# Kernel optimization log

Hardware: AMD Instinct MI355X
Metric: run time of the kernel (lower is better)

## Reference

```python
import jax, jax.numpy as jnp
import numpy as np

Y_DIM = 2
Z_DIM = 128
EPS = 1e-08


def setup_inputs() -> dict:
    key = jax.random.key(0)
    k1, k2, k3, k4 = jax.random.split(key, 4)
    b, n, m, x_dim = 8, 1024, 2048, 1
    c = Y_DIM + 1
    x = jax.random.normal(k1, (b, n, x_dim), dtype=jnp.float32)
    y = jax.random.normal(k2, (b, n, Y_DIM), dtype=jnp.float32)
    t = jax.random.normal(k3, (b, m, x_dim), dtype=jnp.float32)
    # learned params
    sigma = jnp.zeros((c,), dtype=jnp.float32)  # log(length_scale=1) = 0
    W = jax.random.normal(k4, (Z_DIM, c), dtype=jnp.float32) * 0.05
    b_fc = jnp.zeros((Z_DIM,), dtype=jnp.float32)
    return {"x": x, "y": y, "t": t, "sigma": sigma, "W": W, "b_fc": b_fc}


def reference(x, y, t, sigma, W, b_fc):
    # rbf_kernel: diff summed over x_dim -> (b, n, m)
    diff = jnp.sum(t[:, None, :, :] - x[:, :, None, :], axis=-1)  # (b,n,m)
    scale = jnp.exp(sigma)  # (c,)
    # kernel: (b,n,m,c)
    kernel = jnp.exp(-0.5 * (diff[..., None] / scale) ** 2)
    # z = [density=1, y] broadcast-multiplied by kernel, summed over n
    b_, n_, _ = y.shape
    feats = jnp.concatenate([jnp.ones((b_, n_, 1), dtype=y.dtype), y], axis=-1)  # (b,n,c)
    z = jnp.einsum("bnc,bnmc->bmc", feats, kernel)  # (b,m,c)
    density = z[..., :1]
    normalized = z[..., 1:] / (density + EPS)
    z = jnp.concatenate([density, normalized], axis=-1)  # (b,m,c)
    return z @ W.T + b_fc  # (b,m,z_dim)
```

## Files before the change

### kernel.cpp

```cpp
#include <hip/hip_runtime.h>
#include <hip/hip_bf16.h>

constexpr int B  = 8;
constexpr int N  = 1024;
constexpr int M  = 2048;
constexpr int ZD = 128;
constexpr int JPW = 2;
constexpr int JPB = 4 * JPW;
constexpr float EPS = 1e-8f;
constexpr float LOG2E = 1.4426950408889634f;

__global__ __launch_bounds__(256, 8) void encoder_fused(
    const float* __restrict__ x,
    const float* __restrict__ y,
    const float* __restrict__ t,
    const float* __restrict__ sigma,
    const float* __restrict__ W,
    const float* __restrict__ bfc,
    float* __restrict__ out)
{
    __shared__ float sx[N];
    __shared__ float sy1[N];
    __shared__ float sy2[N];

    const int blk  = blockIdx.x;
    const int b    = blk / (M / JPB);
    const int jt   = blk % (M / JPB);
    const int tid  = threadIdx.x;
    const int wave = tid >> 6;
    const int lane = tid & 63;

    for (int i = tid; i < N; i += 256) {
        sx[i] = x[b * N + i];
        float2 yv = reinterpret_cast<const float2*>(y)[b * N + i];
        sy1[i] = yv.x;
        sy2[i] = yv.y;
    }
    __syncthreads();

    const float s0 = sigma[0], s1 = sigma[1], s2 = sigma[2];
    const float q0 = -0.5f * LOG2E * __builtin_amdgcn_exp2f(-2.0f * s0 * LOG2E);
    const float q1 = -0.5f * LOG2E * __builtin_amdgcn_exp2f(-2.0f * s1 * LOG2E);
    const float q2 = -0.5f * LOG2E * __builtin_amdgcn_exp2f(-2.0f * s2 * LOG2E);

    const int j0 = jt * JPB + wave * JPW;
    const float ta = t[b * M + j0];
    const float tb = t[b * M + j0 + 1];

    float z0a = 0.f, z1a = 0.f, z2a = 0.f;
    float z0b = 0.f, z1b = 0.f, z2b = 0.f;

    if (s0 == s1 && s1 == s2) {
#pragma unroll
        for (int k = 0; k < N / 64; ++k) {
            const int i = k * 64 + lane;
            const float xi = sx[i], y1 = sy1[i], y2 = sy2[i];
            const float da = ta - xi, db = tb - xi;
            const float ea = __builtin_amdgcn_exp2f(da * da * q0);
            const float eb = __builtin_amdgcn_exp2f(db * db * q0);
            z0a += ea;  z1a = fmaf(y1, ea, z1a);  z2a = fmaf(y2, ea, z2a);
            z0b += eb;  z1b = fmaf(y1, eb, z1b);  z2b = fmaf(y2, eb, z2b);
        }
    } else {
#pragma unroll
        for (int k = 0; k < N / 64; ++k) {
            const int i = k * 64 + lane;
            const float xi = sx[i], y1 = sy1[i], y2 = sy2[i];
            const float da = ta - xi, db = tb - xi;
            const float da2 = da * da, db2 = db * db;
            z0a += __builtin_amdgcn_exp2f(da2 * q0);
            z1a = fmaf(y1, __builtin_amdgcn_exp2f(da2 * q1), z1a);
            z2a = fmaf(y2, __builtin_amdgcn_exp2f(da2 * q2), z2a);
            z0b += __builtin_amdgcn_exp2f(db2 * q0);
            z1b = fmaf(y1, __builtin_amdgcn_exp2f(db2 * q1), z1b);
            z2b = fmaf(y2, __builtin_amdgcn_exp2f(db2 * q2), z2b);
        }
    }

#pragma unroll
    for (int off = 32; off; off >>= 1) {
        z0a += __shfl_xor(z0a, off);
        z1a += __shfl_xor(z1a, off);
        z2a += __shfl_xor(z2a, off);
        z0b += __shfl_xor(z0b, off);
        z1b += __shfl_xor(z1b, off);
        z2b += __shfl_xor(z2b, off);
    }

    const float inva = 1.0f / (z0a + EPS);
    const float a1 = z1a * inva, a2 = z2a * inva;
    const float invb = 1.0f / (z0b + EPS);
    const float b1 = z1b * invb, b2 = z2b * invb;

    const int k0 = lane * 2;
    const float w00 = W[k0 * 3 + 0], w01 = W[k0 * 3 + 1], w02 = W[k0 * 3 + 2];
    const float w10 = W[(k0 + 1) * 3 + 0], w11 = W[(k0 + 1) * 3 + 1], w12 = W[(k0 + 1) * 3 + 2];
    const float bf0 = bfc[k0], bf1 = bfc[k0 + 1];

    float2 oa, ob;
    oa.x = fmaf(z0a, w00, fmaf(a1, w01, fmaf(a2, w02, bf0)));
    oa.y = fmaf(z0a, w10, fmaf(a1, w11, fmaf(a2, w12, bf1)));
    ob.x = fmaf(z0b, w00, fmaf(b1, w01, fmaf(b2, w02, bf0)));
    ob.y = fmaf(z0b, w10, fmaf(b1, w11, fmaf(b2, w12, bf1)));

    reinterpret_cast<float2*>(out)[(size_t)(b * M + j0) * (ZD / 2) + lane]       = oa;
    reinterpret_cast<float2*>(out)[(size_t)(b * M + j0 + 1) * (ZD / 2) + lane]   = ob;
}

extern "C" void kernel_launch(void* const* d_in, const int* in_sizes, int n_in,
                              void* d_out, int out_size, void* d_ws, size_t ws_size,
                              hipStream_t stream) {
    const float* x     = (const float*)d_in[0];
    const float* y     = (const float*)d_in[1];
    const float* t     = (const float*)d_in[2];
    const float* sigma = (const float*)d_in[3];
    const float* W     = (const float*)d_in[4];
    const float* bfc   = (const float*)d_in[5];
    float* out = (float*)d_out;

    dim3 grid(B * (M / JPB));
    encoder_fused<<<grid, 256, 0, stream>>>(x, y, t, sigma, W, bfc, out);
}
```

Measured before the change: 72.12 us.

## Prescale x and t by sqrt of kernel coefficient and process four targets per wave

Each wave now handles four target points instead of two. This halves the grid and amortizes every shared-memory load of x and y over more exp evaluations. In the uniform-sigma path, x and t are prescaled by sqrt(-q0), so the exponent becomes -(d*d) and a multiply per element is removed. The cost is more accumulator registers, fewer blocks for latency hiding, and slightly different rounding from the prescaling.

```diff
diff --git a/kernel.cpp b/kernel.cpp
--- a/kernel.cpp
+++ b/kernel.cpp
@@ -5,7 +5,7 @@
 constexpr int N  = 1024;
 constexpr int M  = 2048;
 constexpr int ZD = 128;
-constexpr int JPW = 2;
+constexpr int JPW = 4;
 constexpr int JPB = 4 * JPW;
 constexpr float EPS = 1e-8f;
 constexpr float LOG2E = 1.4426950408889634f;
@@ -30,81 +30,85 @@
     const int wave = tid >> 6;
     const int lane = tid & 63;
 
+    const float s0 = sigma[0], s1 = sigma[1], s2 = sigma[2];
+    const float q0 = -0.5f * LOG2E * __builtin_amdgcn_exp2f(-2.0f * s0 * LOG2E);
+    const float q1 = -0.5f * LOG2E * __builtin_amdgcn_exp2f(-2.0f * s1 * LOG2E);
+    const float q2 = -0.5f * LOG2E * __builtin_amdgcn_exp2f(-2.0f * s2 * LOG2E);
+
+    const bool uniform = (s0 == s1) && (s1 == s2);
+    const float sc = uniform ? __builtin_amdgcn_sqrtf(-q0) : 1.0f;
+
     for (int i = tid; i < N; i += 256) {
-        sx[i] = x[b * N + i];
+        sx[i] = x[b * N + i] * sc;
         float2 yv = reinterpret_cast<const float2*>(y)[b * N + i];
         sy1[i] = yv.x;
         sy2[i] = yv.y;
     }
     __syncthreads();
 
-    const float s0 = sigma[0], s1 = sigma[1], s2 = sigma[2];
-    const float q0 = -0.5f * LOG2E * __builtin_amdgcn_exp2f(-2.0f * s0 * LOG2E);
-    const float q1 = -0.5f * LOG2E * __builtin_amdgcn_exp2f(-2.0f * s1 * LOG2E);
-    const float q2 = -0.5f * LOG2E * __builtin_amdgcn_exp2f(-2.0f * s2 * LOG2E);
+    const int j0 = jt * JPB + wave * JPW;
+    float tj[JPW];
+#pragma unroll
+    for (int r = 0; r < JPW; ++r) tj[r] = t[b * M + j0 + r] * sc;
 
-    const int j0 = jt * JPB + wave * JPW;
-    const float ta = t[b * M + j0];
-    const float tb = t[b * M + j0 + 1];
+    float z0[JPW] = {0.f, 0.f, 0.f, 0.f};
+    float z1[JPW] = {0.f, 0.f, 0.f, 0.f};
+    float z2[JPW] = {0.f, 0.f, 0.f, 0.f};
 
-    float z0a = 0.f, z1a = 0.f, z2a = 0.f;
-    float z0b = 0.f, z1b = 0.f, z2b = 0.f;
-
-    if (s0 == s1 && s1 == s2) {
+    if (uniform) {
 #pragma unroll
         for (int k = 0; k < N / 64; ++k) {
             const int i = k * 64 + lane;
             const float xi = sx[i], y1 = sy1[i], y2 = sy2[i];
-            const float da = ta - xi, db = tb - xi;
-            const float ea = __builtin_amdgcn_exp2f(da * da * q0);
-            const float eb = __builtin_amdgcn_exp2f(db * db * q0);
-            z0a += ea;  z1a = fmaf(y1, ea, z1a);  z2a = fmaf(y2, ea, z2a);
-            z0b += eb;  z1b = fmaf(y1, eb, z1b);  z2b = fmaf(y2, eb, z2b);
+#pragma unroll
+            for (int r = 0; r < JPW; ++r) {
+                const float d = tj[r] - xi;
+                const float e = __builtin_amdgcn_exp2f(-(d * d));
+                z0[r] += e;
+                z1[r] = fmaf(y1, e, z1[r]);
+                z2[r] = fmaf(y2, e, z2[r]);
+            }
         }
     } else {
 #pragma unroll
         for (int k = 0; k < N / 64; ++k) {
             const int i = k * 64 + lane;
             const float xi = sx[i], y1 = sy1[i], y2 = sy2[i];
-            const float da = ta - xi, db = tb - xi;
-            const float da2 = da * da, db2 = db * db;
-            z0a += __builtin_amdgcn_exp2f(da2 * q0);
-            z1a = fmaf(y1, __builtin_amdgcn_exp2f(da2 * q1), z1a);
-            z2a = fmaf(y2, __builtin_amdgcn_exp2f(da2 * q2), z2a);
-            z0b += __builtin_amdgcn_exp2f(db2 * q0);
-            z1b = fmaf(y1, __builtin_amdgcn_exp2f(db2 * q1), z1b);
-            z2b = fmaf(y2, __builtin_amdgcn_exp2f(db2 * q2), z2b);
+#pragma unroll
+            for (int r = 0; r < JPW; ++r) {
+                const float d  = tj[r] - xi;
+                const float d2 = d * d;
+                z0[r] += __builtin_amdgcn_exp2f(d2 * q0);
+                z1[r] = fmaf(y1, __builtin_amdgcn_exp2f(d2 * q1), z1[r]);
+                z2[r] = fmaf(y2, __builtin_amdgcn_exp2f(d2 * q2), z2[r]);
+            }
         }
     }
 
 #pragma unroll
     for (int off = 32; off; off >>= 1) {
-        z0a += __shfl_xor(z0a, off);
-        z1a += __shfl_xor(z1a, off);
-        z2a += __shfl_xor(z2a, off);
-        z0b += __shfl_xor(z0b, off);
-        z1b += __shfl_xor(z1b, off);
-        z2b += __shfl_xor(z2b, off);
+#pragma unroll
+        for (int r = 0; r < JPW; ++r) {
+            z0[r] += __shfl_xor(z0[r], off);
+            z1[r] += __shfl_xor(z1[r], off);
+            z2[r] += __shfl_xor(z2[r], off);
+        }
     }
-
-    const float inva = 1.0f / (z0a + EPS);
-    const float a1 = z1a * inva, a2 = z2a * inva;
-    const float invb = 1.0f / (z0b + EPS);
-    const float b1 = z1b * invb, b2 = z2b * invb;
 
     const int k0 = lane * 2;
     const float w00 = W[k0 * 3 + 0], w01 = W[k0 * 3 + 1], w02 = W[k0 * 3 + 2];
     const float w10 = W[(k0 + 1) * 3 + 0], w11 = W[(k0 + 1) * 3 + 1], w12 = W[(k0 + 1) * 3 + 2];
     const float bf0 = bfc[k0], bf1 = bfc[k0 + 1];
 
-    float2 oa, ob;
-    oa.x = fmaf(z0a, w00, fmaf(a1, w01, fmaf(a2, w02, bf0)));
-    oa.y = fmaf(z0a, w10, fmaf(a1, w11, fmaf(a2, w12, bf1)));
-    ob.x = fmaf(z0b, w00, fmaf(b1, w01, fmaf(b2, w02, bf0)));
-    ob.y = fmaf(z0b, w10, fmaf(b1, w11, fmaf(b2, w12, bf1)));
-
-    reinterpret_cast<float2*>(out)[(size_t)(b * M + j0) * (ZD / 2) + lane]       = oa;
-    reinterpret_cast<float2*>(out)[(size_t)(b * M + j0 + 1) * (ZD / 2) + lane]   = ob;
+#pragma unroll
+    for (int r = 0; r < JPW; ++r) {
+        const float inv = 1.0f / (z0[r] + EPS);
+        const float a1 = z1[r] * inv, a2 = z2[r] * inv;
+        float2 o;
+        o.x = fmaf(z0[r], w00, fmaf(a1, w01, fmaf(a2, w02, bf0)));
+        o.y = fmaf(z0[r], w10, fmaf(a1, w11, fmaf(a2, w12, bf1)));
+        reinterpret_cast<float2*>(out)[(size_t)(b * M + j0 + r) * (ZD / 2) + lane] = o;
+    }
 }
 
 extern "C" void kernel_launch(void* const* d_in, const int* in_sizes, int n_in,
```

Result: slower. 85.71 us (+18.9%).
